# Kernel optimization log

Measured on AMD Instinct MI355X. Metric: run time of the kernel, lower is better.

Reference implementation:

```python
import jax, jax.numpy as jnp
import numpy as np

P = 8    # patch_size
N = 16   # n_patches
WS = 32  # window_size


def setup_inputs() -> dict:
    key = jax.random.key(0)
    k1, k2 = jax.random.split(key)
    B, C, H, W = 8, 12, 512, 512
    return {
        "data_real": jax.random.normal(k1, (B, C, H, W), dtype=jnp.float32),
        "data_imag": jax.random.normal(k2, (B, C, H, W), dtype=jnp.float32),
        "ref_x": 248,
        "ref_y": 248,
    }


def reference(data_real, data_imag, ref_x, ref_y):
    p, n, ws = P, N, WS
    # complex64 represented as trailing real/imag axis (matches torch.view_as_real)
    data = jnp.stack([data_real, data_imag], axis=-1)  # [B,C,H,W,2]
    B, C, H, W, _ = data.shape

    # reference patch at (ref_x, ref_y)
    ref = data[:, :, ref_x:ref_x + p, ref_y:ref_y + p, :]  # [B,C,p,p,2]

    # clamped search window (static Python ints -> static shapes)
    wx0 = max(ref_x - ws // 2, 0); wx1 = min(ref_x + ws // 2, H)
    wy0 = max(ref_y - ws // 2, 0); wy1 = min(ref_y + ws // 2, W)
    win = data[:, :, wx0:wx1, wy0:wy1, :]  # [B,C,Wh,Ww,2]
    Wh, Ww = win.shape[2], win.shape[3]
    Ph, Pw = Wh - p + 1, Ww - p + 1

    # all sliding patches in the window, vectorized via fancy indexing
    ix = jnp.arange(Ph)[:, None] + jnp.arange(p)[None, :]  # [Ph,p]
    iy = jnp.arange(Pw)[:, None] + jnp.arange(p)[None, :]  # [Pw,p]
    patches = win[:, :, ix[:, None, :, None], iy[None, :, None, :], :]  # [B,C,Ph,Pw,p,p,2]

    # mse_loss over view_as_real == 0.5 * mean(|diff|^2) over p*p complex elems
    diff = patches - ref[:, :, None, None]
    dists = 0.5 * jnp.mean(diff * diff, axis=(-3, -2, -1))  # [B,C,Ph,Pw]

    M = Ph * Pw  # row-major (x outer, y inner) matches the torch loop order
    dists = dists.reshape(B, C, M)
    pats = patches.reshape(B, C, M, p * p, 2)

    slot = jnp.arange(n)

    def select(dv, pv):  # dv: [M], pv: [M, p*p, 2]
        def step(carry, inp):
            nd, ns = carry
            di, pi = inp
            mask = nd > di                      # candidate slots
            oh = (slot == jnp.argmax(mask)) & jnp.any(mask)  # first True slot
            nd = jnp.where(oh, di, nd)
            ns = jnp.where(oh[:, None, None], pi, ns)
            return (nd, ns), None

        init = (jnp.full((n,), 1e33, dtype=dv.dtype),
                jnp.zeros((n, p * p, 2), dtype=pv.dtype))
        (nd, ns), _ = jax.lax.scan(step, init, (dv, pv))
        return ns

    # independent sequential top-n insertion per (batch, contrast)
    sims = jax.vmap(jax.vmap(select))(dists, pats)  # [B,C,n,p*p,2]
    return sims
```

## Files before the change

### kernel.cpp

```cpp
#include <hip/hip_runtime.h>
#include <math.h>

#define PP    8
#define NSEL  16
#define WSZ   32

__global__ __launch_bounds__(256) void patches_select_kernel(
    const float* __restrict__ d_re,
    const float* __restrict__ d_im,
    const int*   __restrict__ p_rx,
    const int*   __restrict__ p_ry,
    float*       __restrict__ out,
    int H, int W)
{
    const int bc   = blockIdx.x;
    const int tid  = threadIdx.x;
    const int lane = tid & 63;

    const int rx = p_rx[0];
    const int ry = p_ry[0];
    const int wx0 = max(rx - WSZ / 2, 0);
    const int wx1 = min(rx + WSZ / 2, H);
    const int wy0 = max(ry - WSZ / 2, 0);
    const int wy1 = min(ry + WSZ / 2, W);
    const int Wh = wx1 - wx0;
    const int Ww = wy1 - wy0;
    const int Ph = Wh - PP + 1;
    const int Pw = Ww - PP + 1;
    const int M  = Ph * Pw;
    const int Mpad = (M + 15) & ~15;

    __shared__ __align__(16) float sre[WSZ][WSZ];
    __shared__ __align__(16) float sim_[WSZ][WSZ];
    __shared__ __align__(16) float sref[PP * PP * 2];
    __shared__ float dists[WSZ * WSZ];

    const size_t plane = (size_t)H * W;
    const float* baseR = d_re + (size_t)bc * plane;
    const float* baseI = d_im + (size_t)bc * plane;

    if (Wh == WSZ && Ww == WSZ && ((wy0 & 3) == 0) && ((W & 3) == 0)) {
        const int nv = WSZ * (WSZ / 4);
        for (int t = tid; t < nv; t += 256) {
            const int i = t >> 3, j4 = (t & 7) << 2;
            const size_t g = (size_t)(wx0 + i) * W + (wy0 + j4);
            *(float4*)&sre[i][j4]  = *(const float4*)&baseR[g];
            *(float4*)&sim_[i][j4] = *(const float4*)&baseI[g];
        }
    } else {
        for (int t = tid; t < Wh * Ww; t += 256) {
            const int i = t / Ww, j = t - i * Ww;
            const size_t g = (size_t)(wx0 + i) * W + (wy0 + j);
            sre[i][j]  = baseR[g];
            sim_[i][j] = baseI[g];
        }
    }
    for (int t = tid; t < PP * PP; t += 256) {
        const int i = t / PP, j = t - i * PP;
        const size_t g = (size_t)(rx + i) * W + (ry + j);
        sref[t * 2 + 0] = baseR[g];
        sref[t * 2 + 1] = baseI[g];
    }
    if (tid < 16 && M + tid < Mpad) dists[M + tid] = INFINITY;
    __syncthreads();

    {
        int nm = 0;
        int mlist[3], mpi[3], mpj[3];
        for (int m = tid; m < M; m += 256) {
            mlist[nm] = m; mpi[nm] = m / Pw; mpj[nm] = m - (m / Pw) * Pw; ++nm;
        }
        float acc[3][8];
#pragma unroll
        for (int mm = 0; mm < 3; ++mm)
#pragma unroll
            for (int j = 0; j < 8; ++j) acc[mm][j] = 0.0f;

        const float4* ref4 = (const float4*)sref;
#pragma unroll
        for (int k = 0; k < 16; ++k) {
            const float4 ra = ref4[2 * k];
            const float4 rb = ref4[2 * k + 1];
            const int dx  = k >> 1;
            const int dyb = (k & 1) * 4;
            for (int mm = 0; mm < nm; ++mm) {
                const float* wr = &sre[mpi[mm] + dx][mpj[mm] + dyb];
                const float* wi = &sim_[mpi[mm] + dx][mpj[mm] + dyb];
                const float w0 = wr[0], w1 = wr[1], w2 = wr[2], w3 = wr[3];
                const float v0 = wi[0], v1 = wi[1], v2 = wi[2], v3 = wi[3];
                float d;
                d = __fsub_rn(w0, ra.x); acc[mm][0] = __fadd_rn(acc[mm][0], __fmul_rn(d, d));
                d = __fsub_rn(v0, ra.y); acc[mm][1] = __fadd_rn(acc[mm][1], __fmul_rn(d, d));
                d = __fsub_rn(w1, ra.z); acc[mm][2] = __fadd_rn(acc[mm][2], __fmul_rn(d, d));
                d = __fsub_rn(v1, ra.w); acc[mm][3] = __fadd_rn(acc[mm][3], __fmul_rn(d, d));
                d = __fsub_rn(w2, rb.x); acc[mm][4] = __fadd_rn(acc[mm][4], __fmul_rn(d, d));
                d = __fsub_rn(v2, rb.y); acc[mm][5] = __fadd_rn(acc[mm][5], __fmul_rn(d, d));
                d = __fsub_rn(w3, rb.z); acc[mm][6] = __fadd_rn(acc[mm][6], __fmul_rn(d, d));
                d = __fsub_rn(v3, rb.w); acc[mm][7] = __fadd_rn(acc[mm][7], __fmul_rn(d, d));
            }
        }
        for (int mm = 0; mm < nm; ++mm) {
            const float s0 = __fadd_rn(__fadd_rn(acc[mm][0], acc[mm][1]),
                                       __fadd_rn(acc[mm][2], acc[mm][3]));
            const float s1 = __fadd_rn(__fadd_rn(acc[mm][4], acc[mm][5]),
                                       __fadd_rn(acc[mm][6], acc[mm][7]));
            const float S  = __fadd_rn(s0, s1);
            dists[mlist[mm]] = S * (1.0f / 256.0f);
        }
    }
    __syncthreads();

    float nd = (lane < NSEL) ? 1e33f : -1.0f;
    int   mi = -1;
    {
        float cur[16];
#pragma unroll
        for (int u = 0; u < 16; ++u) cur[u] = dists[u];
        for (int m0 = 0; m0 < Mpad; m0 += 16) {
            float nxt[16];
            const int nb = m0 + 16;
            if (nb < Mpad) {
#pragma unroll
                for (int u = 0; u < 16; ++u) nxt[u] = dists[nb + u];
            } else {
#pragma unroll
                for (int u = 0; u < 16; ++u) nxt[u] = INFINITY;
            }
#pragma unroll
            for (int u = 0; u < 16; ++u) {
                const unsigned long long mask = __ballot(nd > cur[u]);
                const int first = __ffsll(mask) - 1;
                if (lane == first) { nd = cur[u]; mi = m0 + u; }
            }
#pragma unroll
            for (int u = 0; u < 16; ++u) cur[u] = nxt[u];
        }
    }

    const int slot = tid >> 4;
    const int m = __shfl(mi, slot);
    float* obase = out + (size_t)bc * (NSEL * PP * PP * 2) + tid * 8;
    const int rem0 = (tid & 15) * 8;
    float vals[8];
    if (m >= 0) {
        const int pi = m / Pw, pj = m - (m / Pw) * Pw;
#pragma unroll
        for (int q = 0; q < 8; ++q) {
            const int e = rem0 + q;
            const int kk = e >> 1, comp = e & 1;
            const int dx = kk >> 3, dy = kk & 7;
            vals[q] = comp ? sim_[pi + dx][pj + dy] : sre[pi + dx][pj + dy];
        }
    } else {
#pragma unroll
        for (int q = 0; q < 8; ++q) vals[q] = 0.0f;
    }
    *(float4*)&obase[0] = make_float4(vals[0], vals[1], vals[2], vals[3]);
    *(float4*)&obase[4] = make_float4(vals[4], vals[5], vals[6], vals[7]);
}

extern "C" void kernel_launch(void* const* d_in, const int* in_sizes, int n_in,
                              void* d_out, int out_size, void* d_ws, size_t ws_size,
                              hipStream_t stream) {
    const float* d_re = (const float*)d_in[0];
    const float* d_im = (const float*)d_in[1];
    const int*   p_rx = (const int*)d_in[2];
    const int*   p_ry = (const int*)d_in[3];
    float* out = (float*)d_out;

    const int H = 512, W = 512;
    const int BC = in_sizes[0] / (H * W);

    patches_select_kernel<<<BC, 256, 0, stream>>>(d_re, d_im, p_rx, p_ry, out, H, W);
}
```

Baseline: 242.3 us.

## Skip non-improving blocks in top-n selection and unroll fixed distance loop

The sequential top-16 insertion now runs on a single wavefront instead of every wave repeating it. Each block of 16 distances is skipped when its minimum is not below the largest kept value (slot 15, which the insertion order keeps as the maximum). This removes most of the per-element ballot work. The distance stage now gives each thread exactly three clamped patch positions with precomputed pointers instead of a runtime-sized list loop, which should help register allocation and unrolling. Selected indices are passed to the output stage through shared memory instead of a shuffle.

Result: faster. 196.7 us (-18.8%).

```diff
diff --git a/kernel.cpp b/kernel.cpp
--- a/kernel.cpp
+++ b/kernel.cpp
@@ -4,6 +4,22 @@
 #define PP    8
 #define NSEL  16
 #define WSZ   32
+
+#define ACC8(A, WR, WI, OFF) do {                                         \
+    const float _w0 = (WR)[(OFF)+0], _w1 = (WR)[(OFF)+1];                 \
+    const float _w2 = (WR)[(OFF)+2], _w3 = (WR)[(OFF)+3];                 \
+    const float _v0 = (WI)[(OFF)+0], _v1 = (WI)[(OFF)+1];                 \
+    const float _v2 = (WI)[(OFF)+2], _v3 = (WI)[(OFF)+3];                 \
+    float _d;                                                             \
+    _d = __fsub_rn(_w0, ra.x); A[0] = __fadd_rn(A[0], __fmul_rn(_d,_d));  \
+    _d = __fsub_rn(_v0, ra.y); A[1] = __fadd_rn(A[1], __fmul_rn(_d,_d));  \
+    _d = __fsub_rn(_w1, ra.z); A[2] = __fadd_rn(A[2], __fmul_rn(_d,_d));  \
+    _d = __fsub_rn(_v1, ra.w); A[3] = __fadd_rn(A[3], __fmul_rn(_d,_d));  \
+    _d = __fsub_rn(_w2, rb.x); A[4] = __fadd_rn(A[4], __fmul_rn(_d,_d));  \
+    _d = __fsub_rn(_v2, rb.y); A[5] = __fadd_rn(A[5], __fmul_rn(_d,_d));  \
+    _d = __fsub_rn(_w3, rb.z); A[6] = __fadd_rn(A[6], __fmul_rn(_d,_d));  \
+    _d = __fsub_rn(_v3, rb.w); A[7] = __fadd_rn(A[7], __fmul_rn(_d,_d));  \
+} while (0)
 
 __global__ __launch_bounds__(256) void patches_select_kernel(
     const float* __restrict__ d_re,
@@ -13,9 +29,8 @@
     float*       __restrict__ out,
     int H, int W)
 {
-    const int bc   = blockIdx.x;
-    const int tid  = threadIdx.x;
-    const int lane = tid & 63;
+    const int bc  = blockIdx.x;
+    const int tid = threadIdx.x;
 
     const int rx = p_rx[0];
     const int ry = p_ry[0];
@@ -33,7 +48,8 @@
     __shared__ __align__(16) float sre[WSZ][WSZ];
     __shared__ __align__(16) float sim_[WSZ][WSZ];
     __shared__ __align__(16) float sref[PP * PP * 2];
-    __shared__ float dists[WSZ * WSZ];
+    __shared__ __align__(16) float dists[WSZ * WSZ];
+    __shared__ int selIdx[NSEL];
 
     const size_t plane = (size_t)H * W;
     const float* baseR = d_re + (size_t)bc * plane;
@@ -61,84 +77,93 @@
         sref[t * 2 + 0] = baseR[g];
         sref[t * 2 + 1] = baseI[g];
     }
-    if (tid < 16 && M + tid < Mpad) dists[M + tid] = INFINITY;
+    if (tid < Mpad - M) dists[M + tid] = INFINITY;
     __syncthreads();
 
     {
-        int nm = 0;
-        int mlist[3], mpi[3], mpj[3];
-        for (int m = tid; m < M; m += 256) {
-            mlist[nm] = m; mpi[nm] = m / Pw; mpj[nm] = m - (m / Pw) * Pw; ++nm;
-        }
-        float acc[3][8];
-#pragma unroll
-        for (int mm = 0; mm < 3; ++mm)
-#pragma unroll
-            for (int j = 0; j < 8; ++j) acc[mm][j] = 0.0f;
+        const int m0 = tid, m1 = tid + 256, m2 = tid + 512;
+        const int mc0 = min(m0, M - 1), mc1 = min(m1, M - 1), mc2 = min(m2, M - 1);
+        const int pi0 = mc0 / Pw, pj0 = mc0 - pi0 * Pw;
+        const int pi1 = mc1 / Pw, pj1 = mc1 - pi1 * Pw;
+        const int pi2 = mc2 / Pw, pj2 = mc2 - pi2 * Pw;
+        const float* w0r = &sre[pi0][pj0];  const float* w0i = &sim_[pi0][pj0];
+        const float* w1r = &sre[pi1][pj1];  const float* w1i = &sim_[pi1][pj1];
+        const float* w2r = &sre[pi2][pj2];  const float* w2i = &sim_[pi2][pj2];
+
+        float a0[8], a1[8], a2[8];
+#pragma unroll
+        for (int j = 0; j < 8; ++j) { a0[j] = 0.0f; a1[j] = 0.0f; a2[j] = 0.0f; }
 
         const float4* ref4 = (const float4*)sref;
 #pragma unroll
         for (int k = 0; k < 16; ++k) {
             const float4 ra = ref4[2 * k];
             const float4 rb = ref4[2 * k + 1];
-            const int dx  = k >> 1;
-            const int dyb = (k & 1) * 4;
-            for (int mm = 0; mm < nm; ++mm) {
-                const float* wr = &sre[mpi[mm] + dx][mpj[mm] + dyb];
-                const float* wi = &sim_[mpi[mm] + dx][mpj[mm] + dyb];
-                const float w0 = wr[0], w1 = wr[1], w2 = wr[2], w3 = wr[3];
-                const float v0 = wi[0], v1 = wi[1], v2 = wi[2], v3 = wi[3];
-                float d;
-                d = __fsub_rn(w0, ra.x); acc[mm][0] = __fadd_rn(acc[mm][0], __fmul_rn(d, d));
-                d = __fsub_rn(v0, ra.y); acc[mm][1] = __fadd_rn(acc[mm][1], __fmul_rn(d, d));
-                d = __fsub_rn(w1, ra.z); acc[mm][2] = __fadd_rn(acc[mm][2], __fmul_rn(d, d));
-                d = __fsub_rn(v1, ra.w); acc[mm][3] = __fadd_rn(acc[mm][3], __fmul_rn(d, d));
-                d = __fsub_rn(w2, rb.x); acc[mm][4] = __fadd_rn(acc[mm][4], __fmul_rn(d, d));
-                d = __fsub_rn(v2, rb.y); acc[mm][5] = __fadd_rn(acc[mm][5], __fmul_rn(d, d));
-                d = __fsub_rn(w3, rb.z); acc[mm][6] = __fadd_rn(acc[mm][6], __fmul_rn(d, d));
-                d = __fsub_rn(v3, rb.w); acc[mm][7] = __fadd_rn(acc[mm][7], __fmul_rn(d, d));
+            const int off = (k >> 1) * WSZ + (k & 1) * 4;
+            ACC8(a0, w0r, w0i, off);
+            ACC8(a1, w1r, w1i, off);
+            ACC8(a2, w2r, w2i, off);
+        }
+        {
+            const float s0 = __fadd_rn(__fadd_rn(a0[0], a0[1]), __fadd_rn(a0[2], a0[3]));
+            const float s1 = __fadd_rn(__fadd_rn(a0[4], a0[5]), __fadd_rn(a0[6], a0[7]));
+            if (m0 < M) dists[m0] = __fadd_rn(s0, s1) * (1.0f / 256.0f);
+        }
+        {
+            const float s0 = __fadd_rn(__fadd_rn(a1[0], a1[1]), __fadd_rn(a1[2], a1[3]));
+            const float s1 = __fadd_rn(__fadd_rn(a1[4], a1[5]), __fadd_rn(a1[6], a1[7]));
+            if (m1 < M) dists[m1] = __fadd_rn(s0, s1) * (1.0f / 256.0f);
+        }
+        {
+            const float s0 = __fadd_rn(__fadd_rn(a2[0], a2[1]), __fadd_rn(a2[2], a2[3]));
+            const float s1 = __fadd_rn(__fadd_rn(a2[4], a2[5]), __fadd_rn(a2[6], a2[7]));
+            if (m2 < M) dists[m2] = __fadd_rn(s0, s1) * (1.0f / 256.0f);
+        }
+    }
+    __syncthreads();
+
+    if (tid < 64) {
+        float nd = (tid < NSEL) ? 1e33f : -1.0f;
+        int   mi = -1;
+        float tmax = 1e33f;
+        const float4* d4 = (const float4*)dists;
+        float4 c0 = d4[0], c1 = d4[1], c2 = d4[2], c3 = d4[3];
+        const int NB = Mpad >> 4;
+        for (int b = 0; b < NB; ++b) {
+            float4 n0, n1, n2, n3;
+            if (b + 1 < NB) {
+                n0 = d4[4 * b + 4]; n1 = d4[4 * b + 5];
+                n2 = d4[4 * b + 6]; n3 = d4[4 * b + 7];
+            } else {
+                n0 = n1 = n2 = n3 = make_float4(INFINITY, INFINITY, INFINITY, INFINITY);
             }
-        }
-        for (int mm = 0; mm < nm; ++mm) {
-            const float s0 = __fadd_rn(__fadd_rn(acc[mm][0], acc[mm][1]),
-                                       __fadd_rn(acc[mm][2], acc[mm][3]));
-            const float s1 = __fadd_rn(__fadd_rn(acc[mm][4], acc[mm][5]),
-                                       __fadd_rn(acc[mm][6], acc[mm][7]));
-            const float S  = __fadd_rn(s0, s1);
-            dists[mlist[mm]] = S * (1.0f / 256.0f);
-        }
+            const float bmin =
+                fminf(fminf(fminf(fminf(c0.x, c0.y), fminf(c0.z, c0.w)),
+                            fminf(fminf(c1.x, c1.y), fminf(c1.z, c1.w))),
+                      fminf(fminf(fminf(c2.x, c2.y), fminf(c2.z, c2.w)),
+                            fminf(fminf(c3.x, c3.y), fminf(c3.z, c3.w))));
+            if (bmin < tmax) {
+                const int mb = b << 4;
+                const float cur[16] = { c0.x, c0.y, c0.z, c0.w,
+                                        c1.x, c1.y, c1.z, c1.w,
+                                        c2.x, c2.y, c2.z, c2.w,
+                                        c3.x, c3.y, c3.z, c3.w };
+#pragma unroll
+                for (int u = 0; u < 16; ++u) {
+                    const unsigned long long mask = __ballot(nd > cur[u]);
+                    const int first = __ffsll(mask) - 1;
+                    if (tid == first) { nd = cur[u]; mi = mb + u; }
+                }
+                tmax = __shfl(nd, 15);
+            }
+            c0 = n0; c1 = n1; c2 = n2; c3 = n3;
+        }
+        if (tid < NSEL) selIdx[tid] = mi;
     }
     __syncthreads();
 
-    float nd = (lane < NSEL) ? 1e33f : -1.0f;
-    int   mi = -1;
-    {
-        float cur[16];
-#pragma unroll
-        for (int u = 0; u < 16; ++u) cur[u] = dists[u];
-        for (int m0 = 0; m0 < Mpad; m0 += 16) {
-            float nxt[16];
-            const int nb = m0 + 16;
-            if (nb < Mpad) {
-#pragma unroll
-                for (int u = 0; u < 16; ++u) nxt[u] = dists[nb + u];
-            } else {
-#pragma unroll
-                for (int u = 0; u < 16; ++u) nxt[u] = INFINITY;
-            }
-#pragma unroll
-            for (int u = 0; u < 16; ++u) {
-                const unsigned long long mask = __ballot(nd > cur[u]);
-                const int first = __ffsll(mask) - 1;
-                if (lane == first) { nd = cur[u]; mi = m0 + u; }
-            }
-#pragma unroll
-            for (int u = 0; u < 16; ++u) cur[u] = nxt[u];
-        }
-    }
-
     const int slot = tid >> 4;
-    const int m = __shfl(mi, slot);
+    const int m = selIdx[slot];
     float* obase = out + (size_t)bc * (NSEL * PP * PP * 2) + tid * 8;
     const int rem0 = (tid & 15) * 8;
     float vals[8];
```
